# Kernel optimization log

Measured on AMD Instinct MI355X. Metric: run time of the kernel, lower is better.

Reference implementation:

```python
import jax, jax.numpy as jnp
import numpy as np

E = 8          # num_local_experts
D = 1024       # hidden_size
F = 4096       # intermediate_size_moe
T = 2048       # tokens (seq_len)
K = 2          # num_experts_per_tok


def setup_inputs() -> dict:
    key = jax.random.key(0)
    k_x, k_r, k_g, k_u, k_d = jax.random.split(key, 5)
    s = lambda fan_in: 1.0 / np.sqrt(fan_in)
    return {
        "x_TD": jax.random.normal(k_x, (T, D), dtype=jnp.float32),
        "w_router_DE": jax.random.normal(k_r, (D, E), dtype=jnp.float32) * s(D),
        "kernel_gating_EDF": jax.random.normal(k_g, (E, D, F), dtype=jnp.float32) * s(D),
        "kernel_up_proj_EDF": jax.random.normal(k_u, (E, D, F), dtype=jnp.float32) * s(D),
        "kernel_down_proj_EFD": jax.random.normal(k_d, (E, F, D), dtype=jnp.float32) * s(F),
    }


def reference(x_TD, w_router_DE, kernel_gating_EDF, kernel_up_proj_EDF, kernel_down_proj_EFD):
    # --- Router: softmax -> top-k -> renormalize ---
    logits_TE = x_TD @ w_router_DE                       # [T, E]
    probs_TE = jax.nn.softmax(logits_TE, axis=-1)
    topk_vals, topk_idx = jax.lax.top_k(probs_TE, K)     # [T, K]
    topk_vals = topk_vals / jnp.sum(topk_vals, axis=-1, keepdims=True)  # renormalize=True
    # Dense combine weights: scatter top-k weights back to [T, E]
    weights_TE = jnp.sum(
        jax.nn.one_hot(topk_idx, E, dtype=x_TD.dtype) * topk_vals[..., None], axis=1
    )

    # --- Dense-mat expert MLP (SwiGLU), all experts for all tokens ---
    gate_TEF = jnp.einsum("td,edf->tef", x_TD, kernel_gating_EDF)
    up_TEF = jnp.einsum("td,edf->tef", x_TD, kernel_up_proj_EDF)
    h_TEF = jax.nn.silu(gate_TEF) * up_TEF

    # Down-project each expert and combine weighted by router
    # (apply_expert_weight_before_computation=False -> weight applied at combine)
    out_TD = jnp.einsum("tef,efd,te->td", h_TEF, kernel_down_proj_EFD, weights_TE)
    return out_TD
```

## Files before the change

kernel.cpp:

```cpp
#include <hip/hip_runtime.h>
#include <hip/hip_bf16.h>
#include <math.h>

#define T_TOK 2048
#define D_DIM 1024
#define F_DIM 4096
#define E_NUM 8

typedef __attribute__((ext_vector_type(8))) short short8;
typedef __attribute__((ext_vector_type(4))) short short4v;
typedef __attribute__((ext_vector_type(4))) float floatx4;

__device__ __forceinline__ short f2bf(float f) {
  union { float f; unsigned u; } v; v.f = f;
  unsigned r = v.u + 0x7fffu + ((v.u >> 16) & 1u);
  return (short)(r >> 16);
}

__device__ __forceinline__ void gld_lds16(const void* g, void* l) {
  __builtin_amdgcn_global_load_lds(
      (const __attribute__((address_space(1))) unsigned int*)g,
      (__attribute__((address_space(3))) unsigned int*)l, 16, 0, 0);
}

__global__ __launch_bounds__(256) void router_kernel(
    const float* __restrict__ x, const float* __restrict__ wr,
    int* __restrict__ counts, int* __restrict__ slot_sid, float* __restrict__ slot_w) {
  int lane = threadIdx.x & 63;
  int wave = threadIdx.x >> 6;
  int t = blockIdx.x * 4 + wave;
  const float* xr = x + (size_t)t * D_DIM;
  float acc[8];
#pragma unroll
  for (int e = 0; e < 8; e++) acc[e] = 0.f;
#pragma unroll
  for (int i = 0; i < 16; i++) {
    int d = i * 64 + lane;
    float xv = xr[d];
    const float* w = wr + d * 8;
    float4 w0 = *(const float4*)(w);
    float4 w1 = *(const float4*)(w + 4);
    acc[0] += xv * w0.x; acc[1] += xv * w0.y;
    acc[2] += xv * w0.z; acc[3] += xv * w0.w;
    acc[4] += xv * w1.x; acc[5] += xv * w1.y;
    acc[6] += xv * w1.z; acc[7] += xv * w1.w;
  }
#pragma unroll
  for (int off = 32; off > 0; off >>= 1) {
#pragma unroll
    for (int e = 0; e < 8; e++) acc[e] += __shfl_xor(acc[e], off, 64);
  }
  if (lane == 0) {
    int e1 = 0; float l1 = acc[0];
#pragma unroll
    for (int e = 1; e < 8; e++) { if (acc[e] > l1) { l1 = acc[e]; e1 = e; } }
    int e2 = -1; float l2 = -3.4e38f;
#pragma unroll
    for (int e = 0; e < 8; e++) { if (e != e1 && acc[e] > l2) { l2 = acc[e]; e2 = e; } }
    float w1 = 1.f / (1.f + __expf(l2 - l1));
    float w2 = 1.f - w1;
    int p1 = atomicAdd(&counts[e1], 1);
    slot_sid[e1 * T_TOK + p1] = 2 * t;
    slot_w[e1 * T_TOK + p1] = w1;
    int p2 = atomicAdd(&counts[e2], 1);
    slot_sid[e2 * T_TOK + p2] = 2 * t + 1;
    slot_w[e2 * T_TOK + p2] = w2;
  }
}

__global__ __launch_bounds__(256) void cvt_x_kernel(const float* __restrict__ x,
                                                    short* __restrict__ Xb) {
  int i = blockIdx.x * 256 + threadIdx.x;
  float4 v = ((const float4*)x)[i];
  short4v s;
  s[0] = f2bf(v.x); s[1] = f2bf(v.y); s[2] = f2bf(v.z); s[3] = f2bf(v.w);
  ((short4v*)Xb)[i] = s;
}

__global__ __launch_bounds__(256) void transpose_cvt_kernel(
    const float* __restrict__ src, short* __restrict__ dst, int R, int C) {
  __shared__ short tile[64][68];
  int cb = blockIdx.x * 64, rb = blockIdx.y * 64;
  size_t plane = (size_t)blockIdx.z * R * C;
  src += plane; dst += plane;
  int tid = threadIdx.x;
  int r0 = tid >> 4, c4 = (tid & 15) * 4;
#pragma unroll
  for (int i = 0; i < 4; i++) {
    int r = r0 + i * 16;
    float4 v = *(const float4*)&src[(size_t)(rb + r) * C + cb + c4];
    short4v s;
    s[0] = f2bf(v.x); s[1] = f2bf(v.y); s[2] = f2bf(v.z); s[3] = f2bf(v.w);
    *(short4v*)&tile[r][c4] = s;
  }
  __syncthreads();
  int c0 = tid >> 4, r4 = (tid & 15) * 4;
#pragma unroll
  for (int i = 0; i < 4; i++) {
    int c = c0 + i * 16;
    short4v s;
    s[0] = tile[r4][c]; s[1] = tile[r4 + 1][c];
    s[2] = tile[r4 + 2][c]; s[3] = tile[r4 + 3][c];
    *(short4v*)&dst[(size_t)(cb + c) * R + rb + r4] = s;
  }
}

__global__ __launch_bounds__(256, 3) void gateup_kernel(
    const short* __restrict__ Xb, const short* __restrict__ WgT, const short* __restrict__ WuT,
    const int* __restrict__ counts, const int* __restrict__ slot_sid,
    short* __restrict__ H) {
  __shared__ short smem[8192];
  __shared__ int s_sid[128];

  int bid = blockIdx.x;
  int mt = bid >> 9;
  int e  = (bid >> 6) & 7;
  int nt = bid & 63;
  int n_e = counts[e];
  if (mt * 128 >= n_e) return;

  int tid = threadIdx.x;
  if (tid < 128) {
    int i = mt * 128 + tid;
    if (i > n_e - 1) i = n_e - 1;
    s_sid[tid] = slot_sid[e * T_TOK + i];
  }
  __syncthreads();

  int lane = tid & 63;
  int w = tid >> 6;
  int wm = w >> 1, wn = w & 1;
  int r16 = lane & 15, q = lane >> 4;

  int rl = lane >> 2;
  int kc = (lane & 3) * 8;
  const short* aP0 = Xb + (size_t)(s_sid[w * 16 + rl] >> 1) * D_DIM + kc;
  const short* aP1 = Xb + (size_t)(s_sid[64 + w * 16 + rl] >> 1) * D_DIM + kc;
  size_t wbase = (size_t)e * F_DIM * D_DIM + (size_t)(nt * 64 + w * 16 + rl) * D_DIM;
  const short* gP = WgT + wbase + kc;
  const short* uP = WuT + wbase + kc;
  short* ldsA0 = smem + w * 512;
  short* ldsA1 = smem + 2048 + w * 512;
  short* ldsBg = smem + 4096 + w * 512;
  short* ldsBu = smem + 6144 + w * 512;

  floatx4 zero4 = {0.f, 0.f, 0.f, 0.f};
  floatx4 accg[4][2], accu[4][2];
#pragma unroll
  for (int a = 0; a < 4; a++)
#pragma unroll
    for (int b = 0; b < 2; b++) { accg[a][b] = zero4; accu[a][b] = zero4; }

  for (int kb = 0; kb < D_DIM / 32; kb++) {
    gld_lds16(aP0, ldsA0);
    gld_lds16(aP1, ldsA1);
    gld_lds16(gP, ldsBg);
    gld_lds16(uP, ldsBu);
    aP0 += 32; aP1 += 32; gP += 32; uP += 32;
    __syncthreads();
    const short* As = smem;
    const short* Bg = smem + 4096;
    const short* Bu = smem + 6144;
    short8 af[4], bgf[2], buf_[2];
#pragma unroll
    for (int f = 0; f < 4; f++)
      af[f] = *(const short8*)&As[(wm * 64 + f * 16 + r16) * 32 + q * 8];
#pragma unroll
    for (int f = 0; f < 2; f++) {
      bgf[f]  = *(const short8*)&Bg[(wn * 32 + f * 16 + r16) * 32 + q * 8];
      buf_[f] = *(const short8*)&Bu[(wn * 32 + f * 16 + r16) * 32 + q * 8];
    }
#pragma unroll
    for (int fm = 0; fm < 4; fm++)
#pragma unroll
      for (int fn = 0; fn < 2; fn++) {
        accg[fm][fn] = __builtin_amdgcn_mfma_f32_16x16x32_bf16(af[fm], bgf[fn],  accg[fm][fn], 0, 0, 0);
        accu[fm][fn] = __builtin_amdgcn_mfma_f32_16x16x32_bf16(af[fm], buf_[fn], accu[fm][fn], 0, 0, 0);
      }
    __syncthreads();
  }

  short* slab = smem;
#pragma unroll
  for (int fm = 0; fm < 4; fm++) {
#pragma unroll
    for (int reg = 0; reg < 4; reg++) {
      int rowl = wm * 16 + q * 4 + reg;
#pragma unroll
      for (int fn = 0; fn < 2; fn++) {
        float g = accg[fm][fn][reg];
        float u = accu[fm][fn][reg];
        float h = g * u / (1.f + __expf(-g));
        slab[rowl * 72 + wn * 32 + fn * 16 + r16] = f2bf(h);
      }
    }
    __syncthreads();
    int rr = tid >> 3, cs = (tid & 7) * 8;
    int grow = (rr >> 4) * 64 + fm * 16 + (rr & 15);
    if (mt * 128 + grow < n_e) {
      int sid = s_sid[grow];
      short8 v0 = *(const short8*)&slab[rr * 72 + cs];
      *(short8*)(H + (size_t)sid * F_DIM + nt * 64 + cs) = v0;
    }
    __syncthreads();
  }
}

__global__ __launch_bounds__(256, 3) void down_kernel(
    const short* __restrict__ H, const short* __restrict__ WdT,
    const int* __restrict__ counts, const int* __restrict__ slot_sid,
    const float* __restrict__ slot_w, float* __restrict__ Y) {
  __shared__ short smem[6144];
  __shared__ int s_sid[128];
  __shared__ float s_w[128];

  int bid = blockIdx.x;
  int mt = bid >> 9;
  int e  = (bid >> 6) & 7;
  int sk = (bid >> 4) & 3;
  int nt = bid & 15;
  int n_e = counts[e];
  if (mt * 128 >= n_e) return;

  int tid = threadIdx.x;
  if (tid < 128) {
    int i = mt * 128 + tid;
    if (i > n_e - 1) i = n_e - 1;
    s_sid[tid] = slot_sid[e * T_TOK + i];
    s_w[tid]   = slot_w[e * T_TOK + i];
  }
  __syncthreads();

  int lane = tid & 63;
  int w = tid >> 6;
  int wm = w >> 1, wn = w & 1;
  int r16 = lane & 15, q = lane >> 4;

  int rl = lane >> 2;
  int kc = (lane & 3) * 8;
  int ks = sk * (F_DIM / 4);
  const short* aP0 = H + (size_t)s_sid[w * 16 + rl] * F_DIM + ks + kc;
  const short* aP1 = H + (size_t)s_sid[64 + w * 16 + rl] * F_DIM + ks + kc;
  const short* bP = WdT + ((size_t)e * D_DIM + nt * 64 + w * 16 + rl) * F_DIM + ks + kc;
  short* ldsA0 = smem + w * 512;
  short* ldsA1 = smem + 2048 + w * 512;
  short* ldsB  = smem + 4096 + w * 512;

  floatx4 zero4 = {0.f, 0.f, 0.f, 0.f};
  floatx4 acc[4][2];
#pragma unroll
  for (int a = 0; a < 4; a++)
#pragma unroll
    for (int b = 0; b < 2; b++) acc[a][b] = zero4;

  for (int kb = 0; kb < (F_DIM / 4) / 32; kb++) {
    gld_lds16(aP0, ldsA0);
    gld_lds16(aP1, ldsA1);
    gld_lds16(bP, ldsB);
    aP0 += 32; aP1 += 32; bP += 32;
    __syncthreads();
    const short* As = smem;
    const short* Bs = smem + 4096;
    short8 af[4], bf[2];
#pragma unroll
    for (int f = 0; f < 4; f++)
      af[f] = *(const short8*)&As[(wm * 64 + f * 16 + r16) * 32 + q * 8];
#pragma unroll
    for (int f = 0; f < 2; f++)
      bf[f] = *(const short8*)&Bs[(wn * 32 + f * 16 + r16) * 32 + q * 8];
#pragma unroll
    for (int fm = 0; fm < 4; fm++)
#pragma unroll
      for (int fn = 0; fn < 2; fn++)
        acc[fm][fn] = __builtin_amdgcn_mfma_f32_16x16x32_bf16(af[fm], bf[fn], acc[fm][fn], 0, 0, 0);
    __syncthreads();
  }

#pragma unroll
  for (int fm = 0; fm < 4; fm++) {
#pragma unroll
    for (int reg = 0; reg < 4; reg++) {
      int row = wm * 64 + fm * 16 + q * 4 + reg;
      int i = mt * 128 + row;
      if (i < n_e) {
        int sid = s_sid[row];
        float wgt = s_w[row];
        float* yp = Y + ((size_t)sk * (T_TOK * 2) + sid) * D_DIM + nt * 64 + wn * 32 + r16;
#pragma unroll
        for (int fn = 0; fn < 2; fn++)
          yp[fn * 16] = acc[fm][fn][reg] * wgt;
      }
    }
  }
}

__global__ __launch_bounds__(256) void combine_kernel(
    const float* __restrict__ Y, float* __restrict__ out) {
  int idx = blockIdx.x * 256 + threadIdx.x;
  int t = idx >> 8;
  int j = idx & 255;
  const floatx4* Yv = (const floatx4*)Y;
  floatx4 s = {0.f, 0.f, 0.f, 0.f};
#pragma unroll
  for (int sk = 0; sk < 4; sk++) {
    s += Yv[((size_t)sk * (T_TOK * 2) + 2 * t) * 256 + j];
    s += Yv[((size_t)sk * (T_TOK * 2) + 2 * t + 1) * 256 + j];
  }
  ((floatx4*)out)[idx] = s;
}

extern "C" void kernel_launch(void* const* d_in, const int* in_sizes, int n_in,
                              void* d_out, int out_size, void* d_ws, size_t ws_size,
                              hipStream_t stream) {
  const float* x  = (const float*)d_in[0];
  const float* wr = (const float*)d_in[1];
  const float* Wg = (const float*)d_in[2];
  const float* Wu = (const float*)d_in[3];
  const float* Wd = (const float*)d_in[4];
  float* out = (float*)d_out;

  char* ws = (char*)d_ws;
  int*   counts   = (int*)(ws);
  int*   slot_sid = (int*)(ws + 4096);
  float* slot_w   = (float*)(ws + 4096 + 65536);
  short* Xb       = (short*)(ws + 0x40000);
  short* H        = (short*)(ws + 0x800000);
  short* WgT      = (short*)(ws + 0x2800000);
  short* WuT      = (short*)(ws + 0x6800000);
  short* WdT      = WgT;
  float* Y4       = (float*)WuT;

  hipMemsetAsync(counts, 0, E_NUM * sizeof(int), stream);
  router_kernel<<<T_TOK / 4, 256, 0, stream>>>(x, wr, counts, slot_sid, slot_w);
  cvt_x_kernel<<<T_TOK * D_DIM / 4 / 256, 256, 0, stream>>>(x, Xb);
  transpose_cvt_kernel<<<dim3(F_DIM / 64, D_DIM / 64, E_NUM), 256, 0, stream>>>(Wg, WgT, D_DIM, F_DIM);
  transpose_cvt_kernel<<<dim3(F_DIM / 64, D_DIM / 64, E_NUM), 256, 0, stream>>>(Wu, WuT, D_DIM, F_DIM);
  gateup_kernel<<<16 * E_NUM * 64, 256, 0, stream>>>(Xb, WgT, WuT, counts, slot_sid, H);
  transpose_cvt_kernel<<<dim3(D_DIM / 64, F_DIM / 64, E_NUM), 256, 0, stream>>>(Wd, WdT, F_DIM, D_DIM);
  down_kernel<<<16 * E_NUM * 4 * 16, 256, 0, stream>>>(H, WdT, counts, slot_sid, slot_w, Y4);
  combine_kernel<<<T_TOK * D_DIM / 4 / 256, 256, 0, stream>>>(Y4, out);
}
```

Baseline: 679.7 us.

## Compact expert tile schedule, widen transpose tiles with swizzled LDS, raise occupancy

```diff
diff --git a/kernel.cpp b/kernel.cpp
--- a/kernel.cpp
+++ b/kernel.cpp
@@ -6,6 +6,7 @@
 #define D_DIM 1024
 #define F_DIM 4096
 #define E_NUM 8
+#define MAX_TILES 48
 
 typedef __attribute__((ext_vector_type(8))) short short8;
 typedef __attribute__((ext_vector_type(4))) short short4v;
@@ -68,6 +69,18 @@
   }
 }
 
+__global__ __launch_bounds__(64) void schedule_kernel(
+    const int* __restrict__ counts, int* __restrict__ tiles) {
+  if (threadIdx.x == 0) {
+    int n = 0;
+    for (int e = 0; e < E_NUM; e++) {
+      int nt_ = (counts[e] + 127) >> 7;
+      for (int m = 0; m < nt_; m++) tiles[n++] = (e << 8) | m;
+    }
+    for (int i = n; i < MAX_TILES; i++) tiles[i] = -1;
+  }
+}
+
 __global__ __launch_bounds__(256) void cvt_x_kernel(const float* __restrict__ x,
                                                     short* __restrict__ Xb) {
   int i = blockIdx.x * 256 + threadIdx.x;
@@ -79,45 +92,48 @@
 
 __global__ __launch_bounds__(256) void transpose_cvt_kernel(
     const float* __restrict__ src, short* __restrict__ dst, int R, int C) {
-  __shared__ short tile[64][68];
-  int cb = blockIdx.x * 64, rb = blockIdx.y * 64;
+  __shared__ short tileT[64 * 128];
+  int cb = blockIdx.x * 64, rb = blockIdx.y * 128;
   size_t plane = (size_t)blockIdx.z * R * C;
   src += plane; dst += plane;
   int tid = threadIdx.x;
   int r0 = tid >> 4, c4 = (tid & 15) * 4;
 #pragma unroll
-  for (int i = 0; i < 4; i++) {
+  for (int i = 0; i < 8; i++) {
     int r = r0 + i * 16;
     float4 v = *(const float4*)&src[(size_t)(rb + r) * C + cb + c4];
-    short4v s;
-    s[0] = f2bf(v.x); s[1] = f2bf(v.y); s[2] = f2bf(v.z); s[3] = f2bf(v.w);
-    *(short4v*)&tile[r][c4] = s;
+    int rhw = ((r >> 3) << 3);
+    int rlo = r & 7;
+    tileT[(c4 + 0) * 128 + (((r >> 3) ^ ((c4 + 0) & 15)) << 3) + rlo] = f2bf(v.x);
+    tileT[(c4 + 1) * 128 + (((r >> 3) ^ ((c4 + 1) & 15)) << 3) + rlo] = f2bf(v.y);
+    tileT[(c4 + 2) * 128 + (((r >> 3) ^ ((c4 + 2) & 15)) << 3) + rlo] = f2bf(v.z);
+    tileT[(c4 + 3) * 128 + (((r >> 3) ^ ((c4 + 3) & 15)) << 3) + rlo] = f2bf(v.w);
+    (void)rhw;
   }
   __syncthreads();
-  int c0 = tid >> 4, r4 = (tid & 15) * 4;
+  int c0 = tid >> 4, rq = tid & 15;
 #pragma unroll
   for (int i = 0; i < 4; i++) {
     int c = c0 + i * 16;
-    short4v s;
-    s[0] = tile[r4][c]; s[1] = tile[r4 + 1][c];
-    s[2] = tile[r4 + 2][c]; s[3] = tile[r4 + 3][c];
-    *(short4v*)&dst[(size_t)(cb + c) * R + rb + r4] = s;
-  }
-}
-
-__global__ __launch_bounds__(256, 3) void gateup_kernel(
+    short8 s = *(const short8*)&tileT[c * 128 + ((rq ^ (c & 15)) << 3)];
+    *(short8*)&dst[(size_t)(cb + c) * R + rb + rq * 8] = s;
+  }
+}
+
+__global__ __launch_bounds__(256, 4) void gateup_kernel(
     const short* __restrict__ Xb, const short* __restrict__ WgT, const short* __restrict__ WuT,
     const int* __restrict__ counts, const int* __restrict__ slot_sid,
-    short* __restrict__ H) {
+    const int* __restrict__ tiles, short* __restrict__ H) {
   __shared__ short smem[8192];
   __shared__ int s_sid[128];
 
   int bid = blockIdx.x;
-  int mt = bid >> 9;
-  int e  = (bid >> 6) & 7;
+  int tile = tiles[bid >> 6];
+  if (tile < 0) return;
+  int e  = tile >> 8;
+  int mt = tile & 255;
   int nt = bid & 63;
   int n_e = counts[e];
-  if (mt * 128 >= n_e) return;
 
   int tid = threadIdx.x;
   if (tid < 128) {
@@ -206,21 +222,23 @@
   }
 }
 
-__global__ __launch_bounds__(256, 3) void down_kernel(
+__global__ __launch_bounds__(256, 4) void down_kernel(
     const short* __restrict__ H, const short* __restrict__ WdT,
     const int* __restrict__ counts, const int* __restrict__ slot_sid,
-    const float* __restrict__ slot_w, float* __restrict__ Y) {
+    const float* __restrict__ slot_w, const int* __restrict__ tiles,
+    float* __restrict__ Y) {
   __shared__ short smem[6144];
   __shared__ int s_sid[128];
   __shared__ float s_w[128];
 
   int bid = blockIdx.x;
-  int mt = bid >> 9;
-  int e  = (bid >> 6) & 7;
+  int tile = tiles[bid >> 6];
+  if (tile < 0) return;
+  int e  = tile >> 8;
+  int mt = tile & 255;
   int sk = (bid >> 4) & 3;
   int nt = bid & 15;
   int n_e = counts[e];
-  if (mt * 128 >= n_e) return;
 
   int tid = threadIdx.x;
   if (tid < 128) {
@@ -321,6 +339,7 @@
 
   char* ws = (char*)d_ws;
   int*   counts   = (int*)(ws);
+  int*   tiles    = (int*)(ws + 2048);
   int*   slot_sid = (int*)(ws + 4096);
   float* slot_w   = (float*)(ws + 4096 + 65536);
   short* Xb       = (short*)(ws + 0x40000);
@@ -332,11 +351,12 @@
 
   hipMemsetAsync(counts, 0, E_NUM * sizeof(int), stream);
   router_kernel<<<T_TOK / 4, 256, 0, stream>>>(x, wr, counts, slot_sid, slot_w);
+  schedule_kernel<<<1, 64, 0, stream>>>(counts, tiles);
   cvt_x_kernel<<<T_TOK * D_DIM / 4 / 256, 256, 0, stream>>>(x, Xb);
-  transpose_cvt_kernel<<<dim3(F_DIM / 64, D_DIM / 64, E_NUM), 256, 0, stream>>>(Wg, WgT, D_DIM, F_DIM);
-  transpose_cvt_kernel<<<dim3(F_DIM / 64, D_DIM / 64, E_NUM), 256, 0, stream>>>(Wu, WuT, D_DIM, F_DIM);
-  gateup_kernel<<<16 * E_NUM * 64, 256, 0, stream>>>(Xb, WgT, WuT, counts, slot_sid, H);
-  transpose_cvt_kernel<<<dim3(D_DIM / 64, F_DIM / 64, E_NUM), 256, 0, stream>>>(Wd, WdT, F_DIM, D_DIM);
-  down_kernel<<<16 * E_NUM * 4 * 16, 256, 0, stream>>>(H, WdT, counts, slot_sid, slot_w, Y4);
+  transpose_cvt_kernel<<<dim3(F_DIM / 64, D_DIM / 128, E_NUM), 256, 0, stream>>>(Wg, WgT, D_DIM, F_DIM);
+  transpose_cvt_kernel<<<dim3(F_DIM / 64, D_DIM / 128, E_NUM), 256, 0, stream>>>(Wu, WuT, D_DIM, F_DIM);
+  gateup_kernel<<<MAX_TILES * 64, 256, 0, stream>>>(Xb, WgT, WuT, counts, slot_sid, tiles, H);
+  transpose_cvt_kernel<<<dim3(D_DIM / 64, F_DIM / 128, E_NUM), 256, 0, stream>>>(Wd, WdT, F_DIM, D_DIM);
+  down_kernel<<<MAX_TILES * 64, 256, 0, stream>>>(H, WdT, counts, slot_sid, slot_w, tiles, Y4);
   combine_kernel<<<T_TOK * D_DIM / 4 / 256, 256, 0, stream>>>(Y4, out);
 }
```

Measured after the change: 643.8 us. 5.3% less time.
